# Kernel tuning notes

Measured on AMD Instinct MI355X. Metric: run time of the kernel, lower is better.

## Reference

```python
import jax, jax.numpy as jnp
import numpy as np

BETA = 1.0  # NormEMAVectorQuantizer beta

def l2norm(x, axis=-1, eps=1e-12):
    # matches torch F.normalize(p=2)
    n = jnp.sqrt(jnp.sum(x * x, axis=axis, keepdims=True))
    return x / jnp.maximum(n, eps)


def setup_inputs() -> dict:
    key = jax.random.key(0)
    k1, k2, k3, k4 = jax.random.split(key, 4)
    B, N, D, E, K = 16, 1024, 768, 32, 8192
    features = jax.random.normal(k1, (B, N, D), dtype=jnp.float32)
    # encode_task_layer: Linear(D,D) -> Tanh -> Linear(D,E), trunc_normal std=0.02, zero bias
    W1 = jax.random.normal(k2, (D, D), dtype=jnp.float32) * 0.02
    b1 = jnp.zeros((D,), dtype=jnp.float32)
    W2 = jax.random.normal(k3, (D, E), dtype=jnp.float32) * 0.02
    b2 = jnp.zeros((E,), dtype=jnp.float32)
    # EmbeddingEMA codebook is kept L2-normalized (norm_ema_inplace)
    codebook = l2norm(jax.random.normal(k4, (K, E), dtype=jnp.float32))
    return {"features": features, "W1": W1, "b1": b1, "W2": W2, "b2": b2,
            "codebook": codebook}


def reference(features, W1, b1, W2, b2, codebook):
    B, N, D = features.shape
    E = W2.shape[1]
    # encode_task_layer (fp32, as in torch autocast(enabled=False))
    h = jnp.tanh(features @ W1 + b1) @ W2 + b2          # [B, N, E]
    # NormEMAVectorQuantizer forward
    z = l2norm(h)                                       # [B, N, E]
    zf = z.reshape(-1, E)                               # [B*N, E]
    # squared-distance matrix to codebook
    d = (jnp.sum(zf * zf, axis=1, keepdims=True)
         + jnp.sum(codebook * codebook, axis=1)
         - 2.0 * zf @ codebook.T)                       # [B*N, K]
    idx = jnp.argmin(d, axis=1)                         # [B*N]
    z_q = codebook[idx].reshape(B, N, E)                # gather
    # commitment loss: beta * mse(stop_grad(z_q), z)
    loss = BETA * jnp.mean(jnp.square(jax.lax.stop_gradient(z_q) - z))
    # straight-through estimator
    z_q = z + jax.lax.stop_gradient(z_q - z)
    return z_q, loss, idx.reshape(B, N)
```

## Files before the change

kernel.cpp:

```cpp
#include <hip/hip_runtime.h>
#include <cstdint>

static constexpr int M = 16384;
static constexpr int D = 768;
static constexpr int E = 32;
static constexpr int K = 8192;

typedef _Float16 half8 __attribute__((ext_vector_type(8)));
typedef float f32x4 __attribute__((ext_vector_type(4)));

typedef __attribute__((address_space(1))) const uint32_t gu32;
typedef __attribute__((address_space(3))) uint32_t lu32;
__device__ __forceinline__ void g2l16(const void* g, void* l) {
  __builtin_amdgcn_global_load_lds((gu32*)g, (lu32*)l, 16, 0, 0);
}

__global__ __launch_bounds__(256) void split_w1t(const float* __restrict__ W1,
    _Float16* __restrict__ W1aT, _Float16* __restrict__ W1bT)
{
  __shared__ float tile[32][33];
  const int tx = threadIdx.x & 31, ty = threadIdx.x >> 5;
  const int kb = blockIdx.x * 32, nb = blockIdx.y * 32;
#pragma unroll
  for (int i = 0; i < 4; ++i)
    tile[ty * 4 + i][tx] = W1[(size_t)(kb + ty * 4 + i) * 768 + nb + tx];
  __syncthreads();
#pragma unroll
  for (int i = 0; i < 4; ++i) {
    const int n = nb + ty * 4 + i, k = kb + tx;
    const float v = tile[tx][ty * 4 + i] * 64.0f;
    const _Float16 h = (_Float16)v;
    W1aT[(size_t)n * 768 + k] = h;
    W1bT[(size_t)n * 768 + k] = (_Float16)((v - (float)h) * 4096.0f);
  }
}

__global__ __launch_bounds__(256) void cb_prep(const float* __restrict__ CB,
    float* __restrict__ cc, _Float16* __restrict__ CBh, _Float16* __restrict__ CBr)
{
  const int k = blockIdx.x * 256 + threadIdx.x;
  const float4* p = (const float4*)(CB + (size_t)k * E);
  _Float16 hb[32], rb[32];
  float s = 0.f;
#pragma unroll
  for (int q = 0; q < 8; ++q) {
    float4 v = p[q];
    const float e[4] = {v.x, v.y, v.z, v.w};
#pragma unroll
    for (int j = 0; j < 4; ++j) {
      s += e[j] * e[j];
      const _Float16 h = (_Float16)e[j];
      hb[q * 4 + j] = h;
      rb[q * 4 + j] = (_Float16)((e[j] - (float)h) * 4096.0f);
    }
  }
  cc[k] = s;
#pragma unroll
  for (int q = 0; q < 4; ++q) {
    *(half8*)(CBh + (size_t)k * E + q * 8) = *(half8*)&hb[q * 8];
    *(half8*)(CBr + (size_t)k * E + q * 8) = *(half8*)&rb[q * 8];
  }
}

__global__ __launch_bounds__(256, 2) void gemm1_mfma(
    const float* __restrict__ X, const _Float16* __restrict__ Bag,
    const _Float16* __restrict__ Bbg, const float* __restrict__ bias,
    float* __restrict__ C)
{
  __shared__ __align__(16) char smem[65536];
  constexpr int AaO = 0, AbO = 8192, BaO = 16384, BbO = 24576, BUF = 32768;

  const int t = threadIdx.x;
  const int lane = t & 63;
  const int wave = t >> 6;
  const int wm = wave >> 1, wn = wave & 1;
  const int rowBase = blockIdx.x * 128;
  const int colBase = blockIdx.y * 128;

  const int r0 = t >> 2, s0 = t & 3;
  const float* Xp0 = X + (size_t)(rowBase + r0) * D + s0 * 8;
  const float* Xp1 = X + (size_t)(rowBase + 64 + r0) * D + s0 * 8;
  const _Float16* BaP0 = Bag + (size_t)(colBase + r0) * D + s0 * 8;
  const _Float16* BaP1 = Bag + (size_t)(colBase + 64 + r0) * D + s0 * 8;
  const _Float16* BbP0 = Bbg + (size_t)(colBase + r0) * D + s0 * 8;
  const _Float16* BbP1 = Bbg + (size_t)(colBase + 64 + r0) * D + s0 * 8;
  const int ldsU0 = t * 16, ldsU1 = (256 + t) * 16;

  const int fragA = (wm * 64 + (lane & 15)) * 64 + (lane >> 4) * 16;
  const int fragB = (wn * 64 + (lane & 15)) * 64 + (lane >> 4) * 16;

  f32x4 accM[4][4], accR[4][4];
  const f32x4 z4 = {0.f, 0.f, 0.f, 0.f};
#pragma unroll
  for (int i = 0; i < 4; ++i)
#pragma unroll
    for (int j = 0; j < 4; ++j) { accM[i][j] = z4; accR[i][j] = z4; }

  auto cvtWrite = [&](char* buf, float4 pa, float4 pb, int off) {
    half8 hi, re;
    const float v[8] = {pa.x, pa.y, pa.z, pa.w, pb.x, pb.y, pb.z, pb.w};
#pragma unroll
    for (int e = 0; e < 8; ++e) {
      const _Float16 h = (_Float16)v[e];
      hi[e] = h;
      re[e] = (_Float16)((v[e] - (float)h) * 4096.0f);
    }
    *(half8*)(buf + AaO + off) = hi;
    *(half8*)(buf + AbO + off) = re;
  };
  auto stageB = [&](char* buf, int k0) {
    g2l16(BaP0 + k0, buf + BaO + ldsU0);
    g2l16(BaP1 + k0, buf + BaO + ldsU1);
    g2l16(BbP0 + k0, buf + BbO + ldsU0);
    g2l16(BbP1 + k0, buf + BbO + ldsU1);
  };

  {
    char* buf = smem;
    float4 p00 = *(const float4*)(Xp0);
    float4 p01 = *(const float4*)(Xp0 + 4);
    float4 p10 = *(const float4*)(Xp1);
    float4 p11 = *(const float4*)(Xp1 + 4);
    stageB(buf, 0);
    cvtWrite(buf, p00, p01, ldsU0);
    cvtWrite(buf, p10, p11, ldsU1);
    __syncthreads();
  }

  for (int ks = 0; ks < 24; ++ks) {
    char* bufc = smem + (ks & 1) * BUF;
    char* bufn = smem + ((ks + 1) & 1) * BUF;
    float4 p00, p01, p10, p11;
    const bool pre = (ks < 23);
    if (pre) {
      const int k1 = (ks + 1) * 32;
      p00 = *(const float4*)(Xp0 + k1);
      p01 = *(const float4*)(Xp0 + k1 + 4);
      p10 = *(const float4*)(Xp1 + k1);
      p11 = *(const float4*)(Xp1 + k1 + 4);
      stageB(bufn, k1);
    }
    half8 bAv[4], bBv[4];
#pragma unroll
    for (int fn = 0; fn < 4; ++fn) {
      bAv[fn] = *(const half8*)(bufc + BaO + fragB + fn * 1024);
      bBv[fn] = *(const half8*)(bufc + BbO + fragB + fn * 1024);
    }
#pragma unroll
    for (int fm = 0; fm < 4; ++fm) {
      half8 aA = *(const half8*)(bufc + AaO + fragA + fm * 1024);
      half8 aB = *(const half8*)(bufc + AbO + fragA + fm * 1024);
#pragma unroll
      for (int fn = 0; fn < 4; ++fn) {
        accM[fm][fn] = __builtin_amdgcn_mfma_f32_16x16x32_f16(aA, bAv[fn], accM[fm][fn], 0, 0, 0);
        accR[fm][fn] = __builtin_amdgcn_mfma_f32_16x16x32_f16(aB, bAv[fn], accR[fm][fn], 0, 0, 0);
        accR[fm][fn] = __builtin_amdgcn_mfma_f32_16x16x32_f16(aA, bBv[fn], accR[fm][fn], 0, 0, 0);
      }
    }
    if (pre) {
      cvtWrite(bufn, p00, p01, ldsU0);
      cvtWrite(bufn, p10, p11, ldsU1);
    }
    __syncthreads();
  }

#pragma unroll
  for (int fm = 0; fm < 4; ++fm) {
    const int mb = rowBase + wm * 64 + fm * 16 + (lane >> 4) * 4;
#pragma unroll
    for (int fn = 0; fn < 4; ++fn) {
      const int n = colBase + wn * 64 + fn * 16 + (lane & 15);
      const float bv = bias[n];
#pragma unroll
      for (int r = 0; r < 4; ++r) {
        const float val = accM[fm][fn][r] * 0.015625f
                        + accR[fm][fn][r] * 3.814697265625e-6f + bv;
        C[(size_t)(mb + r) * D + n] = tanhf(val);
      }
    }
  }
}

__global__ __launch_bounds__(256) void gemm2_norm(
    const float* __restrict__ H, const float* __restrict__ W2,
    const float* __restrict__ b2, float* __restrict__ Z)
{
  __shared__ float Hs[32 * 132];
  __shared__ float W2s[128 * 32];
  const int t = threadIdx.x;
  const int rowBase = blockIdx.x * 32;
  const int rl = t >> 3;
  const int n0 = (t & 7) * 4;

  float acc[4] = {0.f, 0.f, 0.f, 0.f};

  for (int kc = 0; kc < D; kc += 128) {
    __syncthreads();
    for (int i = t; i < 32 * 32; i += 256) {
      const int r = i >> 5, gq = i & 31;
      *(float4*)&Hs[r * 132 + gq * 4] =
          *(const float4*)&H[(size_t)(rowBase + r) * D + kc + gq * 4];
    }
    for (int i = t; i < 1024; i += 256)
      *(float4*)&W2s[i * 4] = *(const float4*)&W2[(size_t)kc * E + i * 4];
    __syncthreads();
#pragma unroll 4
    for (int k4 = 0; k4 < 32; ++k4) {
      float4 hv = *(const float4*)&Hs[rl * 132 + k4 * 4];
      const float h[4] = {hv.x, hv.y, hv.z, hv.w};
#pragma unroll
      for (int j = 0; j < 4; ++j) {
        float4 w = *(const float4*)&W2s[(k4 * 4 + j) * E + n0];
        acc[0] = fmaf(h[j], w.x, acc[0]); acc[1] = fmaf(h[j], w.y, acc[1]);
        acc[2] = fmaf(h[j], w.z, acc[2]); acc[3] = fmaf(h[j], w.w, acc[3]);
      }
    }
  }

  float4 bb = *(const float4*)&b2[n0];
  acc[0] += bb.x; acc[1] += bb.y; acc[2] += bb.z; acc[3] += bb.w;
  float ss = acc[0] * acc[0];
  ss += acc[1] * acc[1]; ss += acc[2] * acc[2]; ss += acc[3] * acc[3];
  ss += __shfl_xor(ss, 1, 8);
  ss += __shfl_xor(ss, 2, 8);
  ss += __shfl_xor(ss, 4, 8);
  const float inv = 1.0f / fmaxf(sqrtf(ss), 1e-12f);
  float4 zv = make_float4(acc[0] * inv, acc[1] * inv, acc[2] * inv, acc[3] * inv);
  *(float4*)&Z[(size_t)(rowBase + rl) * E + n0] = zv;
}

__global__ __launch_bounds__(512) void vq_mfma(
    const float* __restrict__ Z, const float* __restrict__ CB,
    const _Float16* __restrict__ CBh, const _Float16* __restrict__ CBr,
    const float* __restrict__ ccg, float* __restrict__ zq_out,
    float* __restrict__ idx_out, float* __restrict__ lossp)
{
  __shared__ float bDs[64][4];
  __shared__ int   bIs[64][4];

  const int t = threadIdx.x;
  const int lane = t & 63, wave = t >> 6;
  const int mh = wave & 1;
  const int cq = wave >> 1;
  const int rowBase = blockIdx.x * 64;
  const int col = lane & 15, kg = lane >> 4;

  half8 zh[2], zr[2];
#pragma unroll
  for (int mt = 0; mt < 2; ++mt) {
    const float* zp = Z + (size_t)(rowBase + mh * 32 + mt * 16 + col) * E + kg * 8;
    const float4 a = *(const float4*)zp;
    const float4 b = *(const float4*)(zp + 4);
    const float v[8] = {a.x, a.y, a.z, a.w, b.x, b.y, b.z, b.w};
#pragma unroll
    for (int e = 0; e < 8; ++e) {
      const _Float16 h = (_Float16)v[e];
      zh[mt][e] = h;
      zr[mt][e] = (_Float16)((v[e] - (float)h) * 4096.0f);
    }
  }

  const f32x4 zero4 = {0.f, 0.f, 0.f, 0.f};
  float best[2][4];
  int bi[2][4];
#pragma unroll
  for (int mt = 0; mt < 2; ++mt)
#pragma unroll
    for (int r = 0; r < 4; ++r) { best[mt][r] = 3.4e38f; bi[mt][r] = 0; }

  const _Float16* ph = CBh + ((size_t)(cq * 2048 + col) * E + kg * 8);
  const _Float16* pr = CBr + ((size_t)(cq * 2048 + col) * E + kg * 8);
  const float* pc = ccg + cq * 2048 + col;
  int curIdx = cq * 2048 + col;

  for (int tt = 0; tt < 128; ++tt) {
    const half8 bh = *(const half8*)ph;
    const half8 br = *(const half8*)pr;
    const float ccv = *pc;
    ph += 16 * E; pr += 16 * E; pc += 16;
#pragma unroll
    for (int mt = 0; mt < 2; ++mt) {
      f32x4 aM = __builtin_amdgcn_mfma_f32_16x16x32_f16(zh[mt], bh, zero4, 0, 0, 0);
      f32x4 aR = __builtin_amdgcn_mfma_f32_16x16x32_f16(zr[mt], bh, zero4, 0, 0, 0);
      aR = __builtin_amdgcn_mfma_f32_16x16x32_f16(zh[mt], br, aR, 0, 0, 0);
#pragma unroll
      for (int r = 0; r < 4; ++r) {
        const float u = fmaf(aR[r], 2.44140625e-4f, aM[r]);
        const float d = fmaf(u, -2.0f, ccv);
        if (d < best[mt][r]) { best[mt][r] = d; bi[mt][r] = curIdx; }
      }
    }
    curIdx += 16;
  }

#pragma unroll
  for (int m = 1; m <= 8; m <<= 1) {
#pragma unroll
    for (int mt = 0; mt < 2; ++mt)
#pragma unroll
      for (int r = 0; r < 4; ++r) {
        const float ob = __shfl_xor(best[mt][r], m, 64);
        const int   oi = __shfl_xor(bi[mt][r],   m, 64);
        if (ob < best[mt][r] || (ob == best[mt][r] && oi < bi[mt][r])) {
          best[mt][r] = ob; bi[mt][r] = oi;
        }
      }
  }

  if (col == 0) {
#pragma unroll
    for (int mt = 0; mt < 2; ++mt)
#pragma unroll
      for (int r = 0; r < 4; ++r) {
        const int rl = mh * 32 + mt * 16 + kg * 4 + r;
        bDs[rl][cq] = best[mt][r];
        bIs[rl][cq] = bi[mt][r];
      }
  }
  __syncthreads();

  const int rl = t >> 3, part = t & 7;
  float bd = bDs[rl][0];
  int bidx = bIs[rl][0];
#pragma unroll
  for (int q = 1; q < 4; ++q)
    if (bDs[rl][q] < bd) { bd = bDs[rl][q]; bidx = bIs[rl][q]; }

  const int row = rowBase + rl;
  const float4 c4 = *(const float4*)&CB[(size_t)bidx * E + part * 4];
  const float4 z4 = *(const float4*)&Z[(size_t)row * E + part * 4];
  const float dx = c4.x - z4.x, dy = c4.y - z4.y;
  const float dz = c4.z - z4.z, dw = c4.w - z4.w;
  *(float4*)&zq_out[(size_t)row * E + part * 4] =
      make_float4(z4.x + dx, z4.y + dy, z4.z + dz, z4.w + dw);
  float ls = dx * dx;
  ls += dy * dy; ls += dz * dz; ls += dw * dw;
  ls += __shfl_xor(ls, 1, 8);
  ls += __shfl_xor(ls, 2, 8);
  ls += __shfl_xor(ls, 4, 8);
  if (part == 0) {
    lossp[row] = ls;
    idx_out[row] = (float)bidx;
  }
}

__global__ __launch_bounds__(256) void loss_reduce(const float* __restrict__ lossp, float* __restrict__ out)
{
  float s = 0.f;
  const float4* p = reinterpret_cast<const float4*>(lossp);
  for (int i = threadIdx.x; i < M / 4; i += 256) {
    float4 v = p[i];
    s += v.x + v.y + v.z + v.w;
  }
#pragma unroll
  for (int m = 32; m >= 1; m >>= 1) s += __shfl_xor(s, m, 64);
  __shared__ float red[4];
  if ((threadIdx.x & 63) == 0) red[threadIdx.x >> 6] = s;
  __syncthreads();
  if (threadIdx.x == 0)
    out[0] = (red[0] + red[1] + red[2] + red[3]) * (1.0f / (float)(M * E));
}

extern "C" void kernel_launch(void* const* d_in, const int* in_sizes, int n_in,
                              void* d_out, int out_size, void* d_ws, size_t ws_size,
                              hipStream_t stream)
{
  const float* X  = (const float*)d_in[0];
  const float* W1 = (const float*)d_in[1];
  const float* b1 = (const float*)d_in[2];
  const float* W2 = (const float*)d_in[3];
  const float* b2 = (const float*)d_in[4];
  const float* CB = (const float*)d_in[5];

  float* out  = (float*)d_out;
  float* zq   = out;
  float* loss = out + 524288;
  float* idxf = out + 524289;

  char* ws = (char*)d_ws;
  float* H1 = (float*)ws;
  float* Z  = (float*)(ws + (size_t)M * D * 4);
  float* cc = Z + (size_t)M * E;
  float* lp = cc + K;
  _Float16* W1aT = (_Float16*)(lp + M);
  _Float16* W1bT = W1aT + (size_t)D * D;
  _Float16* CBh  = W1bT + (size_t)D * D;
  _Float16* CBr  = CBh + (size_t)K * E;

  split_w1t<<<dim3(D / 32, D / 32), 256, 0, stream>>>(W1, W1aT, W1bT);
  cb_prep<<<dim3(K / 256), 256, 0, stream>>>(CB, cc, CBh, CBr);
  gemm1_mfma<<<dim3(M / 128, D / 128), 256, 0, stream>>>(X, W1aT, W1bT, b1, H1);
  gemm2_norm<<<dim3(M / 32), 256, 0, stream>>>(H1, W2, b2, Z);
  vq_mfma<<<dim3(M / 64), 512, 0, stream>>>(Z, CB, CBh, CBr, cc, zq, idxf, lp);
  loss_reduce<<<1, 256, 0, stream>>>(lp, loss);
}
```

Measured before the change: 265.1 us.

## Shrink gemm1 tiles to 64x64 with padded LDS and register-staged loads

Rewrites the split-fp16 GEMM1 kernel to use 64x64 output tiles per block instead of 128x128, with 2x2 MFMA fragments per wave and occupancy hint raised to 4 blocks per CU. The direct global-to-LDS loads for the W1 halves are replaced by register loads followed by LDS stores. The LDS rows are padded to 40 halfs to avoid bank conflicts. The aim is more blocks in flight and fewer LDS conflicts, at the cost of lower data reuse per tile, which means more global traffic for X and W1.

```diff
diff --git a/kernel.cpp b/kernel.cpp
--- a/kernel.cpp
+++ b/kernel.cpp
@@ -8,12 +8,6 @@
 
 typedef _Float16 half8 __attribute__((ext_vector_type(8)));
 typedef float f32x4 __attribute__((ext_vector_type(4)));
-
-typedef __attribute__((address_space(1))) const uint32_t gu32;
-typedef __attribute__((address_space(3))) uint32_t lu32;
-__device__ __forceinline__ void g2l16(const void* g, void* l) {
-  __builtin_amdgcn_global_load_lds((gu32*)g, (lu32*)l, 16, 0, 0);
-}
 
 __global__ __launch_bounds__(256) void split_w1t(const float* __restrict__ W1,
     _Float16* __restrict__ W1aT, _Float16* __restrict__ W1bT)
@@ -62,42 +56,41 @@
   }
 }
 
-__global__ __launch_bounds__(256, 2) void gemm1_mfma(
+__global__ __launch_bounds__(256, 4) void gemm1_mfma(
     const float* __restrict__ X, const _Float16* __restrict__ Bag,
     const _Float16* __restrict__ Bbg, const float* __restrict__ bias,
     float* __restrict__ C)
 {
-  __shared__ __align__(16) char smem[65536];
-  constexpr int AaO = 0, AbO = 8192, BaO = 16384, BbO = 24576, BUF = 32768;
+  constexpr int RS = 40;
+  __shared__ __align__(16) _Float16 Aa[2][64 * RS];
+  __shared__ __align__(16) _Float16 Ab[2][64 * RS];
+  __shared__ __align__(16) _Float16 Ba[2][64 * RS];
+  __shared__ __align__(16) _Float16 Bb[2][64 * RS];
 
   const int t = threadIdx.x;
-  const int lane = t & 63;
-  const int wave = t >> 6;
+  const int lane = t & 63, wave = t >> 6;
   const int wm = wave >> 1, wn = wave & 1;
-  const int rowBase = blockIdx.x * 128;
-  const int colBase = blockIdx.y * 128;
-
-  const int r0 = t >> 2, s0 = t & 3;
-  const float* Xp0 = X + (size_t)(rowBase + r0) * D + s0 * 8;
-  const float* Xp1 = X + (size_t)(rowBase + 64 + r0) * D + s0 * 8;
-  const _Float16* BaP0 = Bag + (size_t)(colBase + r0) * D + s0 * 8;
-  const _Float16* BaP1 = Bag + (size_t)(colBase + 64 + r0) * D + s0 * 8;
-  const _Float16* BbP0 = Bbg + (size_t)(colBase + r0) * D + s0 * 8;
-  const _Float16* BbP1 = Bbg + (size_t)(colBase + 64 + r0) * D + s0 * 8;
-  const int ldsU0 = t * 16, ldsU1 = (256 + t) * 16;
-
-  const int fragA = (wm * 64 + (lane & 15)) * 64 + (lane >> 4) * 16;
-  const int fragB = (wn * 64 + (lane & 15)) * 64 + (lane >> 4) * 16;
-
-  f32x4 accM[4][4], accR[4][4];
+  const int rowBase = blockIdx.x * 64;
+  const int colBase = blockIdx.y * 64;
+
+  const int ra = t >> 2, ka = (t & 3) * 8;
+  const float*    Xp  = X   + (size_t)(rowBase + ra) * D + ka;
+  const _Float16* BaP = Bag + (size_t)(colBase + ra) * D + ka;
+  const _Float16* BbP = Bbg + (size_t)(colBase + ra) * D + ka;
+  const int woff = ra * RS + ka;
+
+  const int arow = wm * 32 + (lane & 15);
+  const int brow = wn * 32 + (lane & 15);
+  const int kg = (lane >> 4) * 8;
+
+  f32x4 accM[2][2], accR[2][2];
   const f32x4 z4 = {0.f, 0.f, 0.f, 0.f};
 #pragma unroll
-  for (int i = 0; i < 4; ++i)
-#pragma unroll
-    for (int j = 0; j < 4; ++j) { accM[i][j] = z4; accR[i][j] = z4; }
-
-  auto cvtWrite = [&](char* buf, float4 pa, float4 pb, int off) {
-    half8 hi, re;
+  for (int i = 0; i < 2; ++i)
+#pragma unroll
+    for (int j = 0; j < 2; ++j) { accM[i][j] = z4; accR[i][j] = z4; }
+
+  auto cvt8 = [](float4 pa, float4 pb, half8& hi, half8& re) {
     const float v[8] = {pa.x, pa.y, pa.z, pa.w, pb.x, pb.y, pb.z, pb.w};
 #pragma unroll
     for (int e = 0; e < 8; ++e) {
@@ -105,71 +98,67 @@
       hi[e] = h;
       re[e] = (_Float16)((v[e] - (float)h) * 4096.0f);
     }
-    *(half8*)(buf + AaO + off) = hi;
-    *(half8*)(buf + AbO + off) = re;
   };
-  auto stageB = [&](char* buf, int k0) {
-    g2l16(BaP0 + k0, buf + BaO + ldsU0);
-    g2l16(BaP1 + k0, buf + BaO + ldsU1);
-    g2l16(BbP0 + k0, buf + BbO + ldsU0);
-    g2l16(BbP1 + k0, buf + BbO + ldsU1);
-  };
 
   {
-    char* buf = smem;
-    float4 p00 = *(const float4*)(Xp0);
-    float4 p01 = *(const float4*)(Xp0 + 4);
-    float4 p10 = *(const float4*)(Xp1);
-    float4 p11 = *(const float4*)(Xp1 + 4);
-    stageB(buf, 0);
-    cvtWrite(buf, p00, p01, ldsU0);
-    cvtWrite(buf, p10, p11, ldsU1);
+    float4 x0 = *(const float4*)Xp;
+    float4 x1 = *(const float4*)(Xp + 4);
+    half8 b0 = *(const half8*)BaP;
+    half8 b1 = *(const half8*)BbP;
+    half8 hi, re;
+    cvt8(x0, x1, hi, re);
+    *(half8*)&Aa[0][woff] = hi;
+    *(half8*)&Ab[0][woff] = re;
+    *(half8*)&Ba[0][woff] = b0;
+    *(half8*)&Bb[0][woff] = b1;
     __syncthreads();
   }
 
   for (int ks = 0; ks < 24; ++ks) {
-    char* bufc = smem + (ks & 1) * BUF;
-    char* bufn = smem + ((ks + 1) & 1) * BUF;
-    float4 p00, p01, p10, p11;
+    const int cur = ks & 1, nxt = cur ^ 1;
     const bool pre = (ks < 23);
+    float4 nx0, nx1;
+    half8 nb0, nb1;
     if (pre) {
       const int k1 = (ks + 1) * 32;
-      p00 = *(const float4*)(Xp0 + k1);
-      p01 = *(const float4*)(Xp0 + k1 + 4);
-      p10 = *(const float4*)(Xp1 + k1);
-      p11 = *(const float4*)(Xp1 + k1 + 4);
-      stageB(bufn, k1);
-    }
-    half8 bAv[4], bBv[4];
-#pragma unroll
-    for (int fn = 0; fn < 4; ++fn) {
-      bAv[fn] = *(const half8*)(bufc + BaO + fragB + fn * 1024);
-      bBv[fn] = *(const half8*)(bufc + BbO + fragB + fn * 1024);
-    }
-#pragma unroll
-    for (int fm = 0; fm < 4; ++fm) {
-      half8 aA = *(const half8*)(bufc + AaO + fragA + fm * 1024);
-      half8 aB = *(const half8*)(bufc + AbO + fragA + fm * 1024);
-#pragma unroll
-      for (int fn = 0; fn < 4; ++fn) {
-        accM[fm][fn] = __builtin_amdgcn_mfma_f32_16x16x32_f16(aA, bAv[fn], accM[fm][fn], 0, 0, 0);
-        accR[fm][fn] = __builtin_amdgcn_mfma_f32_16x16x32_f16(aB, bAv[fn], accR[fm][fn], 0, 0, 0);
-        accR[fm][fn] = __builtin_amdgcn_mfma_f32_16x16x32_f16(aA, bBv[fn], accR[fm][fn], 0, 0, 0);
-      }
-    }
+      nx0 = *(const float4*)(Xp + k1);
+      nx1 = *(const float4*)(Xp + k1 + 4);
+      nb0 = *(const half8*)(BaP + k1);
+      nb1 = *(const half8*)(BbP + k1);
+    }
+    half8 aAv[2], aBv[2], bAv[2], bBv[2];
+#pragma unroll
+    for (int f = 0; f < 2; ++f) {
+      aAv[f] = *(const half8*)&Aa[cur][(arow + f * 16) * RS + kg];
+      aBv[f] = *(const half8*)&Ab[cur][(arow + f * 16) * RS + kg];
+      bAv[f] = *(const half8*)&Ba[cur][(brow + f * 16) * RS + kg];
+      bBv[f] = *(const half8*)&Bb[cur][(brow + f * 16) * RS + kg];
+    }
+#pragma unroll
+    for (int fm = 0; fm < 2; ++fm)
+#pragma unroll
+      for (int fn = 0; fn < 2; ++fn) {
+        accM[fm][fn] = __builtin_amdgcn_mfma_f32_16x16x32_f16(aAv[fm], bAv[fn], accM[fm][fn], 0, 0, 0);
+        accR[fm][fn] = __builtin_amdgcn_mfma_f32_16x16x32_f16(aBv[fm], bAv[fn], accR[fm][fn], 0, 0, 0);
+        accR[fm][fn] = __builtin_amdgcn_mfma_f32_16x16x32_f16(aAv[fm], bBv[fn], accR[fm][fn], 0, 0, 0);
+      }
     if (pre) {
-      cvtWrite(bufn, p00, p01, ldsU0);
-      cvtWrite(bufn, p10, p11, ldsU1);
+      half8 hi, re;
+      cvt8(nx0, nx1, hi, re);
+      *(half8*)&Aa[nxt][woff] = hi;
+      *(half8*)&Ab[nxt][woff] = re;
+      *(half8*)&Ba[nxt][woff] = nb0;
+      *(half8*)&Bb[nxt][woff] = nb1;
     }
     __syncthreads();
   }
 
 #pragma unroll
-  for (int fm = 0; fm < 4; ++fm) {
-    const int mb = rowBase + wm * 64 + fm * 16 + (lane >> 4) * 4;
-#pragma unroll
-    for (int fn = 0; fn < 4; ++fn) {
-      const int n = colBase + wn * 64 + fn * 16 + (lane & 15);
+  for (int fm = 0; fm < 2; ++fm) {
+    const int mb = rowBase + wm * 32 + fm * 16 + (lane >> 4) * 4;
+#pragma unroll
+    for (int fn = 0; fn < 2; ++fn) {
+      const int n = colBase + wn * 32 + fn * 16 + (lane & 15);
       const float bv = bias[n];
 #pragma unroll
       for (int r = 0; r < 4; ++r) {
@@ -389,7 +378,7 @@
 
   split_w1t<<<dim3(D / 32, D / 32), 256, 0, stream>>>(W1, W1aT, W1bT);
   cb_prep<<<dim3(K / 256), 256, 0, stream>>>(CB, cc, CBh, CBr);
-  gemm1_mfma<<<dim3(M / 128, D / 128), 256, 0, stream>>>(X, W1aT, W1bT, b1, H1);
+  gemm1_mfma<<<dim3(M / 64, D / 64), 256, 0, stream>>>(X, W1aT, W1bT, b1, H1);
   gemm2_norm<<<dim3(M / 32), 256, 0, stream>>>(H1, W2, b2, Z);
   vq_mfma<<<dim3(M / 64), 512, 0, stream>>>(Z, CB, CBh, CBr, cc, zq, idxf, lp);
   loss_reduce<<<1, 256, 0, stream>>>(lp, loss);
```

Result: slower. 279.8 us (+5.6%).
